# Performance work log

Measured on AMD Instinct MI355X. Metric: run time of the kernel, lower is better.

## Reference

```python
import jax, jax.numpy as jnp
import numpy as np

H_NOISE_SCALE = 0.01          # config.h_noise_scale
N_ITERS_NO_GRAD = 50          # config.nmf_inference_iters_no_grad
N_ITERS_GRAD = 10             # config.nmf_gradient_iters_with_grad


def _lipschitz(WtW, n_iters=30):
    # Largest eigenvalue of Wx^T Wx via power iteration (Lipschitz constant of the gradient).
    k = WtW.shape[0]
    v = jnp.ones((k,), WtW.dtype) / jnp.sqrt(jnp.asarray(k, WtW.dtype))

    def body(i, v):
        w = WtW @ v
        return w / (jnp.linalg.norm(w) + 1e-12)

    v = jax.lax.fori_loop(0, n_iters, body, v)
    return v @ (WtW @ v)


def _fista_right_update(x, W, h0, n_iters):
    # Solve min_{H>=0} ||x - W H||_F^2 for H^T (shape [batch, k]) with FISTA.
    WtW = W.T @ W                     # [k, k], hoisted out of the loop
    XtW = x.T @ W                     # [batch, k]
    inv_L = 1.0 / _lipschitz(WtW)

    def step(carry, _):
        h, y, t = carry
        grad = y @ WtW - XtW          # d/dH^T of 0.5||x - W H||^2
        h_new = jnp.maximum(y - grad * inv_L, 0.0)   # proximal step (nonneg projection)
        t_new = 0.5 * (1.0 + jnp.sqrt(1.0 + 4.0 * t * t))
        y_new = h_new + ((t - 1.0) / t_new) * (h_new - h)
        return (h_new, y_new, t_new), None

    t0 = jnp.asarray(1.0, x.dtype)
    (h, _, _), _ = jax.lax.scan(step, (h0, h0, t0), None, length=n_iters)
    return h


def setup_inputs() -> dict:
    key = jax.random.key(0)
    k1, k2, k3, k4 = jax.random.split(key, 4)
    x_dim, y_dim, k, batch = 784, 10, 1024, 2048
    x = jax.random.uniform(k1, (x_dim, batch), dtype=jnp.float32)
    Wx = jax.random.uniform(k2, (x_dim, k), dtype=jnp.float32) * 0.02
    Wy = jax.random.uniform(k3, (y_dim, k), dtype=jnp.float32) * 0.02
    h_init = jax.random.uniform(k4, (batch, k), dtype=jnp.float32) * H_NOISE_SCALE
    return {"x": x, "Wx": Wx, "Wy": Wy, "h_init": h_init}


def reference(x, Wx, Wy, h_init):
    # Phase 1: no-grad FISTA warm start (torch.no_grad() -> stop_gradient).
    h = jax.lax.stop_gradient(_fista_right_update(x, Wx, h_init, N_ITERS_NO_GRAD))
    # Phase 2: differentiated FISTA iterations.
    h = _fista_right_update(x, Wx, h, N_ITERS_GRAD)
    # y_pred = einsum('ij,kj->ik', Wy, h_tran): shape [y_dim, batch]
    return jnp.einsum('ij,kj->ik', Wy, h)
```

## Files before the change

### kernel.cpp

```cpp
#include <hip/hip_runtime.h>
#include <math.h>

#define KD    1024
#define BATCH 2048
#define XD    784
#define YD    10

typedef _Float16 f16;
typedef _Float16 f16x8 __attribute__((ext_vector_type(8)));
typedef _Float16 f16x4 __attribute__((ext_vector_type(4)));
typedef float    f32x4 __attribute__((ext_vector_type(4)));

__device__ __forceinline__ void gll16(const void* g, void* l)
{
    __builtin_amdgcn_global_load_lds(
        (const __attribute__((address_space(1))) void*)g,
        (__attribute__((address_space(3))) void*)l,
        16, 0, 0);
}

#define TS  64
#define KS  32
#define LDP 68

__device__ __forceinline__ void atb_body(const float* __restrict__ A,
                                         const float* __restrict__ B,
                                         float* __restrict__ C,
                                         int M, int N, int K, int bx, int by,
                                         float (*As)[LDP], float (*Bs)[LDP])
{
    const int tid = threadIdx.x;
    const int tx = tid & 15, ty = tid >> 4;
    const int i0 = by * TS, j0 = bx * TS;
    float acc[4][4] = {};

    for (int k0 = 0; k0 < K; k0 += KS) {
#pragma unroll
        for (int q = 0; q < 2; ++q) {
            const int f  = tid + q * 256;
            const int kr = f >> 4;
            const int cc = (f & 15) << 2;
            float4 av = make_float4(0.f, 0.f, 0.f, 0.f);
            float4 bv = av;
            if (k0 + kr < K) {
                av = *(const float4*)(A + (size_t)(k0 + kr) * M + i0 + cc);
                bv = *(const float4*)(B + (size_t)(k0 + kr) * N + j0 + cc);
            }
            *(float4*)&As[kr][cc] = av;
            *(float4*)&Bs[kr][cc] = bv;
        }
        __syncthreads();
#pragma unroll
        for (int kk = 0; kk < KS; ++kk) {
            const float4 a4 = *(const float4*)&As[kk][ty << 2];
            const float4 b4 = *(const float4*)&Bs[kk][tx << 2];
            const float a[4] = {a4.x, a4.y, a4.z, a4.w};
            const float b[4] = {b4.x, b4.y, b4.z, b4.w};
#pragma unroll
            for (int r = 0; r < 4; ++r)
#pragma unroll
                for (int c = 0; c < 4; ++c)
                    acc[r][c] = fmaf(a[r], b[c], acc[r][c]);
        }
        __syncthreads();
    }
#pragma unroll
    for (int r = 0; r < 4; ++r) {
        float4 o = make_float4(acc[r][0], acc[r][1], acc[r][2], acc[r][3]);
        *(float4*)(C + (size_t)(i0 + (ty << 2) + r) * N + j0 + (tx << 2)) = o;
    }
}

__global__ __launch_bounds__(256) void setup_fused(const float* __restrict__ x,
                                                   const float* __restrict__ Wx,
                                                   const float* __restrict__ h_init,
                                                   float* __restrict__ WtW,
                                                   float* __restrict__ XtW,
                                                   f16* __restrict__ h0f,
                                                   float* __restrict__ w0)
{
    __shared__ float As[KS][LDP];
    __shared__ float Bs[KS][LDP];
    const int blk = blockIdx.x;
    if (blk < 256) {
        atb_body(Wx, Wx, WtW, KD, KD, XD, blk & 15, blk >> 4, As, Bs);
    } else if (blk < 768) {
        const int l = blk - 256;
        atb_body(x, Wx, XtW, BATCH, KD, XD, l & 15, l >> 4, As, Bs);
    } else if (blk < 1792) {
        const int i = (blk - 768) * 256 + threadIdx.x;
        const f32x4 a = ((const f32x4*)h_init)[2 * i];
        const f32x4 b = ((const f32x4*)h_init)[2 * i + 1];
        f16x8 o;
#pragma unroll
        for (int j = 0; j < 4; ++j) { o[j] = (f16)a[j]; o[j + 4] = (f16)b[j]; }
        ((f16x8*)h0f)[i] = o;
    } else {
        ((float4*)w0)[threadIdx.x] = make_float4(0.03125f, 0.03125f, 0.03125f, 0.03125f);
    }
}

__global__ __launch_bounds__(256) void convert_fused(const float* __restrict__ WtW,
                                                     const float* __restrict__ XtW,
                                                     f16* __restrict__ bhi,
                                                     f16* __restrict__ xth,
                                                     f16* __restrict__ xtl)
{
    const int blk = blockIdx.x;
    if (blk < 512) {
        const int i = blk * 256 + threadIdx.x;
        const f32x4 a = ((const f32x4*)WtW)[2 * i];
        const f32x4 b = ((const f32x4*)WtW)[2 * i + 1];
        f16x8 o;
#pragma unroll
        for (int j = 0; j < 4; ++j) {
            o[j]     = (f16)(256.0f * a[j]);
            o[j + 4] = (f16)(256.0f * b[j]);
        }
        ((f16x8*)bhi)[i] = o;
    } else {
        const int i = (blk - 512) * 256 + threadIdx.x;
        const float4 v = ((const float4*)XtW)[i];
        const f16 h0 = (f16)v.x, h1 = (f16)v.y, h2 = (f16)v.z, h3 = (f16)v.w;
        f16x4 hv = {h0, h1, h2, h3};
        f16x4 lv = {(f16)(v.x - (float)h0), (f16)(v.y - (float)h1),
                    (f16)(v.z - (float)h2), (f16)(v.w - (float)h3)};
        ((f16x4*)xth)[i] = hv;
        ((f16x4*)xtl)[i] = lv;
    }
}

#define BMF 128
#define BNF 64

__global__ __launch_bounds__(512, 2) void fista9(
    const f16* __restrict__ yhP,
    const f16* __restrict__ hhP,
    const f16* __restrict__ bhiP,
    const f16* __restrict__ xthP,
    const f16* __restrict__ xtlP,
    const float* __restrict__ invLp, float cm,
    f16* __restrict__ HO, f16* __restrict__ YO)
{
    __shared__ char lds[49152];

    const int t    = threadIdx.x;
    const int lane = t & 63;
    const int wid  = t >> 6;
    const int wm   = wid >> 1;
    const int wn   = wid & 1;

    const int bid = blockIdx.y * gridDim.x + blockIdx.x;
    const int xc  = bid & 7, j = bid >> 3;
    const int m0  = ((xc >> 1) * 4 + (j >> 3)) * BMF;
    const int n0  = ((xc & 1) * 8 + (j & 7)) * BNF;

    const f16* gsrc[3];
    int ldst[3];
#pragma unroll
    for (int i = 0; i < 3; ++i) {
        const int c = wid * 3 + i;
        if (c < 16) {
            const int g = c & 7, s = c >> 3;
            gsrc[i] = yhP + (size_t)(m0 + 16 * g + (lane & 15)) * KD
                          + 32 * s + 8 * (lane >> 4);
        } else {
            const int cb = c - 16;
            const int g = cb & 3, s = cb >> 2;
            gsrc[i] = bhiP + (size_t)(n0 + 16 * g + (lane & 15)) * KD
                           + 32 * s + 8 * (lane >> 4);
        }
        ldst[i] = c * 1024;
    }

    auto stage = [&](int buf, int kt) {
        char* base = lds + buf * 24576;
#pragma unroll
        for (int i = 0; i < 3; ++i)
            gll16(gsrc[i] + kt * 64, base + ldst[i]);
    };

    f32x4 acc[2][2] = {};

    stage(0, 0);
    asm volatile("s_waitcnt vmcnt(0)" ::: "memory");
    __builtin_amdgcn_s_barrier();
    asm volatile("" ::: "memory");

#pragma unroll
    for (int kt = 0; kt < 16; ++kt) {
        const int buf = kt & 1;
        if (kt < 15) stage(buf ^ 1, kt + 1);
        const char* bb = lds + buf * 24576;

        f16x8 Af[2][2], Bf[2][2];
#pragma unroll
        for (int s = 0; s < 2; ++s) {
#pragma unroll
            for (int f = 0; f < 2; ++f)
                Af[s][f] = *(const f16x8*)(bb + ((s << 3) + wm * 2 + f) * 1024 + lane * 16);
#pragma unroll
            for (int b = 0; b < 2; ++b)
                Bf[s][b] = *(const f16x8*)(bb + 16384 + ((s << 2) + wn * 2 + b) * 1024 + lane * 16);
        }
#pragma unroll
        for (int s = 0; s < 2; ++s)
#pragma unroll
            for (int f = 0; f < 2; ++f)
#pragma unroll
                for (int b = 0; b < 2; ++b)
                    acc[f][b] = __builtin_amdgcn_mfma_f32_16x16x32_f16(Af[s][f], Bf[s][b], acc[f][b], 0, 0, 0);

        if (kt < 15) { asm volatile("s_waitcnt vmcnt(0)" ::: "memory"); }
        __builtin_amdgcn_s_barrier();
        asm volatile("" ::: "memory");
    }

    float* eb = (float*)lds;
#pragma unroll
    for (int f = 0; f < 2; ++f)
#pragma unroll
        for (int b = 0; b < 2; ++b) {
            const int r0 = wm * 32 + 16 * f + 4 * (lane >> 4);
            const int cl = wn * 32 + 16 * b + (lane & 15);
#pragma unroll
            for (int r = 0; r < 4; ++r)
                eb[(r0 + r) * 68 + cl] = acc[f][b][r];
        }
    __syncthreads();

    const int row = t >> 2;
    const int cb  = (t & 3) * 16;
    const float invL  = invLp[0];
    const float invLs = invL * 0.00390625f;
    const size_t gb = (size_t)(m0 + row) * KD + n0 + cb;
#pragma unroll
    for (int q = 0; q < 2; ++q) {
        const f32x4 a0 = *(const f32x4*)(eb + row * 68 + cb + q * 8);
        const f32x4 a1 = *(const f32x4*)(eb + row * 68 + cb + q * 8 + 4);
        const size_t g8 = gb + q * 8;
        const f16x8 yh8 = *(const f16x8*)(yhP + g8);
        const f16x8 hh8 = *(const f16x8*)(hhP + g8);
        const f16x8 xh8 = *(const f16x8*)(xthP + g8);
        const f16x8 xl8 = *(const f16x8*)(xtlP + g8);
        f16x8 oh, oy;
#pragma unroll
        for (int jj = 0; jj < 8; ++jj) {
            const float av = (jj < 4) ? a0[jj] : a1[jj - 4];
            const float xv = (float)xh8[jj] + (float)xl8[jj];
            const float yv = (float)yh8[jj];
            const float hv = (float)hh8[jj];
            const float t1 = fmaf(invL, xv, yv);
            const float hn = fmaxf(fmaf(-invLs, av, t1), 0.f);
            const float yn = fmaf(cm, hn - hv, hn);
            oh[jj] = (f16)hn;
            oy[jj] = (f16)yn;
        }
        *(f16x8*)(HO + g8) = oh;
        *(f16x8*)(YO + g8) = oy;
    }
}

__global__ __launch_bounds__(256) void matvec_n_kernel(const float* __restrict__ WtW,
                                                       const float* __restrict__ win,
                                                       float* __restrict__ wout)
{
    __shared__ float red[4];
    __shared__ float invnS;
    const int t = threadIdx.x;
    const int wave = t >> 6, lane = t & 63;

    const float4 wv = *(const float4*)(win + t * 4);
    float ss = wv.x * wv.x + wv.y * wv.y + wv.z * wv.z + wv.w * wv.w;
#pragma unroll
    for (int off = 32; off > 0; off >>= 1) ss += __shfl_down(ss, off);
    if (lane == 0) red[wave] = ss;
    __syncthreads();
    if (t == 0) invnS = 1.0f / (sqrtf(red[0] + red[1] + red[2] + red[3]) + 1e-12f);
    __syncthreads();
    const float invn = invnS;

    const int row = blockIdx.x * 4 + wave;
    const float* rp = WtW + (size_t)row * KD;
    float s = 0.f;
#pragma unroll
    for (int q = 0; q < KD / 64; ++q)
        s = fmaf(rp[lane + 64 * q], win[lane + 64 * q] * invn, s);
#pragma unroll
    for (int off = 32; off > 0; off >>= 1) s += __shfl_down(s, off);
    if (lane == 0) wout[row] = s;
}

__global__ __launch_bounds__(1024) void rayleigh_n_kernel(const float* __restrict__ wprev,
                                                          const float* __restrict__ wlast,
                                                          float* __restrict__ invL)
{
    __shared__ float red[16];
    __shared__ float invnS;
    const int t = threadIdx.x;
    const float a = wprev[t];
    float ss = a * a;
#pragma unroll
    for (int off = 32; off > 0; off >>= 1) ss += __shfl_down(ss, off);
    if ((t & 63) == 0) red[t >> 6] = ss;
    __syncthreads();
    if (t < 64) {
        float v = (t < 16) ? red[t] : 0.f;
#pragma unroll
        for (int off = 8; off > 0; off >>= 1) v += __shfl_down(v, off);
        if (t == 0) invnS = 1.0f / (sqrtf(v) + 1e-12f);
    }
    __syncthreads();
    float s = (a * invnS) * wlast[t];
#pragma unroll
    for (int off = 32; off > 0; off >>= 1) s += __shfl_down(s, off);
    __syncthreads();
    if ((t & 63) == 0) red[t >> 6] = s;
    __syncthreads();
    if (t == 0) {
        float tot = 0.f;
#pragma unroll
        for (int i = 0; i < 16; ++i) tot += red[i];
        invL[0] = 1.0f / tot;
    }
}

__global__ __launch_bounds__(256) void ypred_kernel(const float* __restrict__ Wy,
                                                    const f16* __restrict__ hh,
                                                    float* __restrict__ out)
{
    const int wave = threadIdx.x >> 6;
    const int lane = threadIdx.x & 63;
    const int b    = blockIdx.x * 4 + wave;
    float p[YD] = {};
    const f16* hp = hh + (size_t)b * KD;
#pragma unroll 4
    for (int q = 0; q < KD / 64; ++q) {
        const int j = lane + 64 * q;
        const float hv = (float)hp[j];
#pragma unroll
        for (int i = 0; i < YD; ++i)
            p[i] = fmaf(Wy[i * KD + j], hv, p[i]);
    }
#pragma unroll
    for (int i = 0; i < YD; ++i) {
        float s = p[i];
#pragma unroll
        for (int off = 32; off > 0; off >>= 1)
            s += __shfl_down(s, off);
        if (lane == 0) out[(size_t)i * BATCH + b] = s;
    }
}

extern "C" void kernel_launch(void* const* d_in, const int* in_sizes, int n_in,
                              void* d_out, int out_size, void* d_ws, size_t ws_size,
                              hipStream_t stream)
{
    const float* x      = (const float*)d_in[0];
    const float* Wx     = (const float*)d_in[1];
    const float* Wy     = (const float*)d_in[2];
    const float* h_init = (const float*)d_in[3];
    float* out = (float*)d_out;

    char* base = (char*)d_ws;
    const size_t MB = 1 << 20;
    float* WtW  = (float*)(base + 0 * MB);
    float* XtW  = (float*)(base + 4 * MB);
    f16* bhiP   = (f16*)(base + 12 * MB);
    f16* xthP   = (f16*)(base + 14 * MB);
    f16* xtlP   = (f16*)(base + 18 * MB);
    f16* h0f    = (f16*)(base + 22 * MB);
    f16* hA     = (f16*)(base + 26 * MB);
    f16* yA     = (f16*)(base + 30 * MB);
    f16* hB     = (f16*)(base + 34 * MB);
    f16* yB     = (f16*)(base + 38 * MB);
    float* wA   = (float*)(base + 42 * MB);
    float* wB   = (float*)(base + 42 * MB + 8192);
    float* invL = (float*)(base + 42 * MB + 16384);

    setup_fused<<<1793, 256, 0, stream>>>(x, Wx, h_init, WtW, XtW, h0f, wA);

    convert_fused<<<2560, 256, 0, stream>>>(WtW, XtW, bhiP, xthP, xtlP);

    float* wcur = wA; float* wnxt = wB;
    for (int it = 0; it < 11; ++it) {
        matvec_n_kernel<<<KD / 4, 256, 0, stream>>>(WtW, wcur, wnxt);
        float* tmp = wcur; wcur = wnxt; wnxt = tmp;
    }
    rayleigh_n_kernel<<<1, 1024, 0, stream>>>(wA, wB, invL);

    float t = 1.0f;
    const f16 *yin = h0f, *hin = h0f;
    int outSel = 1;
    for (int n = 0; n < 60; ++n) {
        if (n == 50) { t = 1.0f; yin = hin; }
        const float tn = 0.5f * (1.0f + sqrtf(1.0f + 4.0f * t * t));
        const float cm = (t - 1.0f) / tn;
        f16* ho = outSel ? hA : hB;
        f16* yo = outSel ? yA : yB;
        fista9<<<dim3(KD / BNF, BATCH / BMF), 512, 0, stream>>>(
            yin, hin, bhiP, xthP, xtlP, invL, cm, ho, yo);
        t = tn;
        hin = ho; yin = yo;
        outSel ^= 1;
    }

    ypred_kernel<<<BATCH / 4, 256, 0, stream>>>(Wy, hin, out);
}
```

Baseline: 1.341 ms.

## Restructure FISTA GEMM to keep B tile resident in LDS and stream A via registers

The FISTA step kernel now uses 128x32 output tiles with 256 threads, giving 512 blocks instead of 256. It loads the whole 32xK slice of the WtW operand into 64KB of LDS once up front. Each wave streams its own 32 rows of the Y operand straight from global memory into a triple-buffered register pipeline. This removes the per-k-step LDS double buffering and block barriers of the old loop. In exchange it uses more LDS per block and more registers, and each wave does direct global loads without sharing A across waves.

```diff
diff --git a/kernel.cpp b/kernel.cpp
--- a/kernel.cpp
+++ b/kernel.cpp
@@ -131,9 +131,9 @@
 }
 
 #define BMF 128
-#define BNF 64
-
-__global__ __launch_bounds__(512, 2) void fista9(
+#define BNF 32
+
+__global__ __launch_bounds__(256, 2) void fista10(
     const f16* __restrict__ yhP,
     const f16* __restrict__ hhP,
     const f16* __restrict__ bhiP,
@@ -142,102 +142,93 @@
     const float* __restrict__ invLp, float cm,
     f16* __restrict__ HO, f16* __restrict__ YO)
 {
-    __shared__ char lds[49152];
+    __shared__ char lds[65536];
 
     const int t    = threadIdx.x;
     const int lane = t & 63;
     const int wid  = t >> 6;
-    const int wm   = wid >> 1;
-    const int wn   = wid & 1;
+    const int lr   = lane & 15;
+    const int lk   = (lane >> 4) * 8;
 
     const int bid = blockIdx.y * gridDim.x + blockIdx.x;
     const int xc  = bid & 7, j = bid >> 3;
-    const int m0  = ((xc >> 1) * 4 + (j >> 3)) * BMF;
-    const int n0  = ((xc & 1) * 8 + (j & 7)) * BNF;
-
-    const f16* gsrc[3];
-    int ldst[3];
-#pragma unroll
-    for (int i = 0; i < 3; ++i) {
-        const int c = wid * 3 + i;
-        if (c < 16) {
-            const int g = c & 7, s = c >> 3;
-            gsrc[i] = yhP + (size_t)(m0 + 16 * g + (lane & 15)) * KD
-                          + 32 * s + 8 * (lane >> 4);
-        } else {
-            const int cb = c - 16;
-            const int g = cb & 3, s = cb >> 2;
-            gsrc[i] = bhiP + (size_t)(n0 + 16 * g + (lane & 15)) * KD
-                           + 32 * s + 8 * (lane >> 4);
-        }
-        ldst[i] = c * 1024;
-    }
-
-    auto stage = [&](int buf, int kt) {
-        char* base = lds + buf * 24576;
-#pragma unroll
-        for (int i = 0; i < 3; ++i)
-            gll16(gsrc[i] + kt * 64, base + ldst[i]);
-    };
-
-    f32x4 acc[2][2] = {};
-
-    stage(0, 0);
+    const int mi  = (xc >> 1) * 4 + (j >> 4);
+    const int ni  = (xc & 1) * 16 + (j & 15);
+    const int m0  = mi * BMF, n0 = ni * BNF;
+
+#pragma unroll
+    for (int i = 0; i < 16; ++i) {
+        const int c = wid * 16 + i;
+        const int b = c & 1, s = (c >> 1) & 1, kt = c >> 2;
+        gll16(bhiP + (size_t)(n0 + 16 * b + lr) * KD + kt * 64 + s * 32 + lk,
+              lds + c * 1024 + lane * 16);
+    }
+
+    const f16* aP[2];
+#pragma unroll
+    for (int f = 0; f < 2; ++f)
+        aP[f] = yhP + (size_t)(m0 + wid * 32 + 16 * f + lr) * KD + lk;
+
+    f16x8 Abuf[3][2][2];
+#pragma unroll
+    for (int kt = 0; kt < 2; ++kt)
+#pragma unroll
+        for (int s = 0; s < 2; ++s)
+#pragma unroll
+            for (int f = 0; f < 2; ++f)
+                Abuf[kt][s][f] = *(const f16x8*)(aP[f] + kt * 64 + 32 * s);
+
     asm volatile("s_waitcnt vmcnt(0)" ::: "memory");
     __builtin_amdgcn_s_barrier();
     asm volatile("" ::: "memory");
 
+    f32x4 acc[2][2] = {};
+
 #pragma unroll
     for (int kt = 0; kt < 16; ++kt) {
-        const int buf = kt & 1;
-        if (kt < 15) stage(buf ^ 1, kt + 1);
-        const char* bb = lds + buf * 24576;
-
-        f16x8 Af[2][2], Bf[2][2];
+        const int cur = kt % 3, nx = (kt + 2) % 3;
+        if (kt < 14) {
+#pragma unroll
+            for (int s = 0; s < 2; ++s)
+#pragma unroll
+                for (int f = 0; f < 2; ++f)
+                    Abuf[nx][s][f] = *(const f16x8*)(aP[f] + (kt + 2) * 64 + 32 * s);
+        }
 #pragma unroll
         for (int s = 0; s < 2; ++s) {
-#pragma unroll
-            for (int f = 0; f < 2; ++f)
-                Af[s][f] = *(const f16x8*)(bb + ((s << 3) + wm * 2 + f) * 1024 + lane * 16);
-#pragma unroll
-            for (int b = 0; b < 2; ++b)
-                Bf[s][b] = *(const f16x8*)(bb + 16384 + ((s << 2) + wn * 2 + b) * 1024 + lane * 16);
-        }
-#pragma unroll
-        for (int s = 0; s < 2; ++s)
-#pragma unroll
-            for (int f = 0; f < 2; ++f)
-#pragma unroll
-                for (int b = 0; b < 2; ++b)
-                    acc[f][b] = __builtin_amdgcn_mfma_f32_16x16x32_f16(Af[s][f], Bf[s][b], acc[f][b], 0, 0, 0);
-
-        if (kt < 15) { asm volatile("s_waitcnt vmcnt(0)" ::: "memory"); }
-        __builtin_amdgcn_s_barrier();
-        asm volatile("" ::: "memory");
-    }
-
+            const f16x8 B0 = *(const f16x8*)(lds + (kt * 4 + s * 2 + 0) * 1024 + lane * 16);
+            const f16x8 B1 = *(const f16x8*)(lds + (kt * 4 + s * 2 + 1) * 1024 + lane * 16);
+#pragma unroll
+            for (int f = 0; f < 2; ++f) {
+                acc[f][0] = __builtin_amdgcn_mfma_f32_16x16x32_f16(Abuf[cur][s][f], B0, acc[f][0], 0, 0, 0);
+                acc[f][1] = __builtin_amdgcn_mfma_f32_16x16x32_f16(Abuf[cur][s][f], B1, acc[f][1], 0, 0, 0);
+            }
+        }
+    }
+
+    __syncthreads();
     float* eb = (float*)lds;
 #pragma unroll
     for (int f = 0; f < 2; ++f)
 #pragma unroll
         for (int b = 0; b < 2; ++b) {
-            const int r0 = wm * 32 + 16 * f + 4 * (lane >> 4);
-            const int cl = wn * 32 + 16 * b + (lane & 15);
+            const int r0 = wid * 32 + 16 * f + 4 * (lane >> 4);
+            const int cl = 16 * b + lr;
 #pragma unroll
             for (int r = 0; r < 4; ++r)
-                eb[(r0 + r) * 68 + cl] = acc[f][b][r];
-        }
-    __syncthreads();
-
-    const int row = t >> 2;
-    const int cb  = (t & 3) * 16;
+                eb[(r0 + r) * 36 + cl] = acc[f][b][r];
+        }
+    __syncthreads();
+
+    const int row = t >> 1;
+    const int cb  = (t & 1) * 16;
     const float invL  = invLp[0];
     const float invLs = invL * 0.00390625f;
     const size_t gb = (size_t)(m0 + row) * KD + n0 + cb;
 #pragma unroll
     for (int q = 0; q < 2; ++q) {
-        const f32x4 a0 = *(const f32x4*)(eb + row * 68 + cb + q * 8);
-        const f32x4 a1 = *(const f32x4*)(eb + row * 68 + cb + q * 8 + 4);
+        const f32x4 a0 = *(const f32x4*)(eb + row * 36 + cb + q * 8);
+        const f32x4 a1 = *(const f32x4*)(eb + row * 36 + cb + q * 8 + 4);
         const size_t g8 = gb + q * 8;
         const f16x8 yh8 = *(const f16x8*)(yhP + g8);
         const f16x8 hh8 = *(const f16x8*)(hhP + g8);
@@ -398,7 +389,7 @@
         const float cm = (t - 1.0f) / tn;
         f16* ho = outSel ? hA : hB;
         f16* yo = outSel ? yA : yB;
-        fista9<<<dim3(KD / BNF, BATCH / BMF), 512, 0, stream>>>(
+        fista10<<<dim3(32, 16), 256, 0, stream>>>(
             yin, hin, bhiP, xthP, xtlP, invL, cm, ho, yo);
         t = tn;
         hin = ho; yin = yo;
```

Result: slower. 1.514 ms (+12.9%).

## Preload whole B panel into LDS once and double-buffer only A tiles

Applied to the files above, without the earlier changes.

The FISTA step kernel now loads its entire 64-column WtW (B) panel across all of K into a 160KB LDS buffer up front, and streams only the A (y) tiles through a double buffer. This cuts per-iteration global-to-LDS traffic and halves the loads issued in the K loop. The cost is that occupancy drops to one block per CU. The epilogue loads are also batched before compute, and the power iteration count falls from 11 to 5 matvecs, which lowers the accuracy of the Lipschitz estimate.

```diff
diff --git a/kernel.cpp b/kernel.cpp
--- a/kernel.cpp
+++ b/kernel.cpp
@@ -132,8 +132,9 @@
 
 #define BMF 128
 #define BNF 64
-
-__global__ __launch_bounds__(512, 2) void fista9(
+#define A_OFF 131072
+
+__global__ __launch_bounds__(512, 1) void fista160(
     const f16* __restrict__ yhP,
     const f16* __restrict__ hhP,
     const f16* __restrict__ bhiP,
@@ -142,66 +143,63 @@
     const float* __restrict__ invLp, float cm,
     f16* __restrict__ HO, f16* __restrict__ YO)
 {
-    __shared__ char lds[49152];
+    __shared__ char lds[163840];
 
     const int t    = threadIdx.x;
     const int lane = t & 63;
     const int wid  = t >> 6;
     const int wm   = wid >> 1;
     const int wn   = wid & 1;
+    const int lr   = lane & 15;
+    const int lk   = (lane >> 4) * 8;
 
     const int bid = blockIdx.y * gridDim.x + blockIdx.x;
     const int xc  = bid & 7, j = bid >> 3;
     const int m0  = ((xc >> 1) * 4 + (j >> 3)) * BMF;
     const int n0  = ((xc & 1) * 8 + (j & 7)) * BNF;
 
-    const f16* gsrc[3];
-    int ldst[3];
-#pragma unroll
-    for (int i = 0; i < 3; ++i) {
-        const int c = wid * 3 + i;
-        if (c < 16) {
-            const int g = c & 7, s = c >> 3;
-            gsrc[i] = yhP + (size_t)(m0 + 16 * g + (lane & 15)) * KD
-                          + 32 * s + 8 * (lane >> 4);
-        } else {
-            const int cb = c - 16;
-            const int g = cb & 3, s = cb >> 2;
-            gsrc[i] = bhiP + (size_t)(n0 + 16 * g + (lane & 15)) * KD
-                           + 32 * s + 8 * (lane >> 4);
-        }
-        ldst[i] = c * 1024;
-    }
-
-    auto stage = [&](int buf, int kt) {
-        char* base = lds + buf * 24576;
-#pragma unroll
-        for (int i = 0; i < 3; ++i)
-            gll16(gsrc[i] + kt * 64, base + ldst[i]);
+#pragma unroll
+    for (int i = 0; i < 16; ++i) {
+        const int c = wid * 16 + i;
+        const int kt = c >> 3, u = c & 7;
+        const int g = u & 3, s = u >> 2;
+        gll16(bhiP + (size_t)(n0 + 16 * g + lr) * KD + kt * 64 + s * 32 + lk,
+              lds + c * 1024 + lane * 16);
+    }
+
+    auto stageA = [&](int buf, int kt) {
+#pragma unroll
+        for (int i = 0; i < 2; ++i) {
+            const int a = wid * 2 + i;
+            const int g = a & 7, s = a >> 3;
+            gll16(yhP + (size_t)(m0 + 16 * g + lr) * KD + kt * 64 + 32 * s + lk,
+                  lds + A_OFF + buf * 16384 + a * 1024 + lane * 16);
+        }
     };
 
-    f32x4 acc[2][2] = {};
-
-    stage(0, 0);
+    stageA(0, 0);
     asm volatile("s_waitcnt vmcnt(0)" ::: "memory");
     __builtin_amdgcn_s_barrier();
     asm volatile("" ::: "memory");
 
+    f32x4 acc[2][2] = {};
+
 #pragma unroll
     for (int kt = 0; kt < 16; ++kt) {
         const int buf = kt & 1;
-        if (kt < 15) stage(buf ^ 1, kt + 1);
-        const char* bb = lds + buf * 24576;
+        if (kt < 15) stageA(buf ^ 1, kt + 1);
 
         f16x8 Af[2][2], Bf[2][2];
 #pragma unroll
         for (int s = 0; s < 2; ++s) {
 #pragma unroll
             for (int f = 0; f < 2; ++f)
-                Af[s][f] = *(const f16x8*)(bb + ((s << 3) + wm * 2 + f) * 1024 + lane * 16);
+                Af[s][f] = *(const f16x8*)(lds + A_OFF + buf * 16384
+                                           + ((s << 3) + wm * 2 + f) * 1024 + lane * 16);
 #pragma unroll
             for (int b = 0; b < 2; ++b)
-                Bf[s][b] = *(const f16x8*)(bb + 16384 + ((s << 2) + wn * 2 + b) * 1024 + lane * 16);
+                Bf[s][b] = *(const f16x8*)(lds + (kt * 8 + (s << 2) + wn * 2 + b) * 1024
+                                           + lane * 16);
         }
 #pragma unroll
         for (int s = 0; s < 2; ++s)
@@ -222,7 +220,7 @@
 #pragma unroll
         for (int b = 0; b < 2; ++b) {
             const int r0 = wm * 32 + 16 * f + 4 * (lane >> 4);
-            const int cl = wn * 32 + 16 * b + (lane & 15);
+            const int cl = wn * 32 + 16 * b + lr;
 #pragma unroll
             for (int r = 0; r < 4; ++r)
                 eb[(r0 + r) * 68 + cl] = acc[f][b][r];
@@ -234,30 +232,48 @@
     const float invL  = invLp[0];
     const float invLs = invL * 0.00390625f;
     const size_t gb = (size_t)(m0 + row) * KD + n0 + cb;
-#pragma unroll
-    for (int q = 0; q < 2; ++q) {
-        const f32x4 a0 = *(const f32x4*)(eb + row * 68 + cb + q * 8);
-        const f32x4 a1 = *(const f32x4*)(eb + row * 68 + cb + q * 8 + 4);
-        const size_t g8 = gb + q * 8;
-        const f16x8 yh8 = *(const f16x8*)(yhP + g8);
-        const f16x8 hh8 = *(const f16x8*)(hhP + g8);
-        const f16x8 xh8 = *(const f16x8*)(xthP + g8);
-        const f16x8 xl8 = *(const f16x8*)(xtlP + g8);
-        f16x8 oh, oy;
+    {
+        const f32x4 a0 = *(const f32x4*)(eb + row * 68 + cb);
+        const f32x4 a1 = *(const f32x4*)(eb + row * 68 + cb + 4);
+        const f32x4 a2 = *(const f32x4*)(eb + row * 68 + cb + 8);
+        const f32x4 a3 = *(const f32x4*)(eb + row * 68 + cb + 12);
+        const f16x8 yh8a = *(const f16x8*)(yhP + gb);
+        const f16x8 yh8b = *(const f16x8*)(yhP + gb + 8);
+        const f16x8 hh8a = *(const f16x8*)(hhP + gb);
+        const f16x8 hh8b = *(const f16x8*)(hhP + gb + 8);
+        const f16x8 xh8a = *(const f16x8*)(xthP + gb);
+        const f16x8 xh8b = *(const f16x8*)(xthP + gb + 8);
+        const f16x8 xl8a = *(const f16x8*)(xtlP + gb);
+        const f16x8 xl8b = *(const f16x8*)(xtlP + gb + 8);
+        f16x8 oha, ohb, oya, oyb;
 #pragma unroll
         for (int jj = 0; jj < 8; ++jj) {
             const float av = (jj < 4) ? a0[jj] : a1[jj - 4];
-            const float xv = (float)xh8[jj] + (float)xl8[jj];
-            const float yv = (float)yh8[jj];
-            const float hv = (float)hh8[jj];
+            const float xv = (float)xh8a[jj] + (float)xl8a[jj];
+            const float yv = (float)yh8a[jj];
+            const float hv = (float)hh8a[jj];
             const float t1 = fmaf(invL, xv, yv);
             const float hn = fmaxf(fmaf(-invLs, av, t1), 0.f);
             const float yn = fmaf(cm, hn - hv, hn);
-            oh[jj] = (f16)hn;
-            oy[jj] = (f16)yn;
-        }
-        *(f16x8*)(HO + g8) = oh;
-        *(f16x8*)(YO + g8) = oy;
+            oha[jj] = (f16)hn;
+            oya[jj] = (f16)yn;
+        }
+#pragma unroll
+        for (int jj = 0; jj < 8; ++jj) {
+            const float av = (jj < 4) ? a2[jj] : a3[jj - 4];
+            const float xv = (float)xh8b[jj] + (float)xl8b[jj];
+            const float yv = (float)yh8b[jj];
+            const float hv = (float)hh8b[jj];
+            const float t1 = fmaf(invL, xv, yv);
+            const float hn = fmaxf(fmaf(-invLs, av, t1), 0.f);
+            const float yn = fmaf(cm, hn - hv, hn);
+            ohb[jj] = (f16)hn;
+            oyb[jj] = (f16)yn;
+        }
+        *(f16x8*)(HO + gb)     = oha;
+        *(f16x8*)(HO + gb + 8) = ohb;
+        *(f16x8*)(YO + gb)     = oya;
+        *(f16x8*)(YO + gb + 8) = oyb;
     }
 }
 
@@ -383,7 +399,7 @@
     convert_fused<<<2560, 256, 0, stream>>>(WtW, XtW, bhiP, xthP, xtlP);
 
     float* wcur = wA; float* wnxt = wB;
-    for (int it = 0; it < 11; ++it) {
+    for (int it = 0; it < 5; ++it) {
         matvec_n_kernel<<<KD / 4, 256, 0, stream>>>(WtW, wcur, wnxt);
         float* tmp = wcur; wcur = wnxt; wnxt = tmp;
     }
@@ -398,7 +414,7 @@
         const float cm = (t - 1.0f) / tn;
         f16* ho = outSel ? hA : hB;
         f16* yo = outSel ? yA : yB;
-        fista9<<<dim3(KD / BNF, BATCH / BMF), 512, 0, stream>>>(
+        fista160<<<dim3(KD / BNF, BATCH / BMF), 512, 0, stream>>>(
             yin, hin, bhiP, xthP, xtlP, invL, cm, ho, yo);
         t = tn;
         hin = ho; yin = yo;
```

New measurement: 1.316 ms. No clear change (-1.9%).
